# Performance work log

Measured on AMD Instinct MI355X. Metric: run time of the kernel, lower is better.

The kernel has to match this reference:

```python
import jax, jax.numpy as jnp
import numpy as np

N = 20000      # nodes
E = 320000     # edges (avg degree 16)
G = 64         # graphs in batch
D_IN = 771     # input feature dim
H = 256        # hidden dim
L = 5          # message-passing layers


def setup_inputs() -> dict:
    key = jax.random.key(0)
    ks = jax.random.split(key, 20)
    s = 0.05  # weight scale (~xavier magnitude)
    f32 = jnp.float32
    return {
        "x": jax.random.normal(ks[0], (N, D_IN), f32),
        "edge_index": jax.random.randint(ks[1], (2, E), 0, N, dtype=jnp.int32),
        "batch": jnp.sort(jax.random.randint(ks[2], (N,), 0, G, dtype=jnp.int32)),
        # input projection
        "proj_w": jax.random.normal(ks[3], (D_IN, H), f32) * s,
        "proj_b": jnp.zeros((H,), f32),
        # GatedGraphConv per-layer message weights [L, H, H]
        "conv_w": jax.random.normal(ks[4], (L, H, H), f32) * s,
        # GRUCell params (torch layout: [3H, H], gates r,z,n)
        "gru_w_ih": jax.random.normal(ks[5], (3 * H, H), f32) * s,
        "gru_w_hh": jax.random.normal(ks[6], (3 * H, H), f32) * s,
        "gru_b_ih": jnp.zeros((3 * H,), f32),
        "gru_b_hh": jnp.zeros((3 * H,), f32),
        # attention pooling MLP
        "att_w1": jax.random.normal(ks[7], (H, H // 2), f32) * s,
        "att_b1": jnp.zeros((H // 2,), f32),
        "att_w2": jax.random.normal(ks[8], (H // 2, 1), f32) * s,
        "att_b2": jnp.zeros((1,), f32),
        # classifier head
        "cls_w1": jax.random.normal(ks[9], (H, H // 2), f32) * s,
        "cls_b1": jnp.zeros((H // 2,), f32),
        "cls_w2": jax.random.normal(ks[10], (H // 2, 1), f32) * s,
        "cls_b2": jnp.zeros((1,), f32),
    }


def reference(x, edge_index, batch, proj_w, proj_b, conv_w,
              gru_w_ih, gru_w_hh, gru_b_ih, gru_b_hh,
              att_w1, att_b1, att_w2, att_b2,
              cls_w1, cls_b1, cls_w2, cls_b2):
    # input projection (+ReLU); dropout disabled (eval mode)
    h = jax.nn.relu(x @ proj_w + proj_b)  # [N, H]
    src, dst = edge_index[0], edge_index[1]

    def step(h, w_i):
        # per-layer linear message, gather at src, scatter-add at dst
        m = h @ w_i                                         # [N, H]
        agg = jax.ops.segment_sum(m[src], dst, num_segments=N)  # [N, H]
        # GRUCell(agg, h)
        gi = agg @ gru_w_ih.T + gru_b_ih                    # [N, 3H]
        gh = h @ gru_w_hh.T + gru_b_hh                      # [N, 3H]
        i_r, i_z, i_n = jnp.split(gi, 3, axis=-1)
        h_r, h_z, h_n = jnp.split(gh, 3, axis=-1)
        r = jax.nn.sigmoid(i_r + h_r)
        z = jax.nn.sigmoid(i_z + h_z)
        n = jnp.tanh(i_n + r * h_n)
        return (1.0 - z) * n + z * h, None

    h, _ = jax.lax.scan(step, h, conv_w)

    # attention pooling = segment softmax over scores, weighted segment sum
    scores = (jnp.tanh(h @ att_w1 + att_b1) @ att_w2 + att_b2)[:, 0]  # [N]
    smax = jax.ops.segment_max(scores, batch, num_segments=G)         # [G]
    e = jnp.exp(scores - smax[batch])
    denom = jax.ops.segment_sum(e, batch, num_segments=G)
    w = e / denom[batch]
    pooled = jax.ops.segment_sum(h * w[:, None], batch, num_segments=G)  # [G, H]

    out = jax.nn.relu(pooled @ cls_w1 + cls_b1) @ cls_w2 + cls_b2  # [G, 1]
    return out[:, 0]
```

## Files before the change

kernel.cpp:

```cpp
#include <hip/hip_runtime.h>
#include <hip/hip_bf16.h>
#include <math.h>

#define N_NODES 20000
#define M_PAD   20096
#define N_EDGES 320000
#define N_GRAPHS 64
#define D_IN 771
#define KP   800
#define HDIM 256
#define L_LAYERS 5

typedef __attribute__((ext_vector_type(8))) short  bf16x8;
typedef __attribute__((ext_vector_type(8))) unsigned short u16x8;
typedef __attribute__((ext_vector_type(4))) float  f32x4;

typedef __attribute__((address_space(3))) void       lds_void;
typedef __attribute__((address_space(1))) const void gconst_void;

__device__ __forceinline__ void gload16(const void* g, void* l) {
    __builtin_amdgcn_global_load_lds((gconst_void*)g, (lds_void*)l, 16, 0, 0);
}

__device__ __forceinline__ unsigned short f2bf(float f) {
    unsigned int u = __float_as_uint(f);
    return (unsigned short)((u + 0x7FFFu + ((u >> 16) & 1u)) >> 16);
}
__device__ __forceinline__ float bf2f(unsigned short h) {
    return __uint_as_float(((unsigned int)h) << 16);
}

__device__ __forceinline__ int swz_src_elems(int lane, int lr) {
    return ((((lane & 3) * 16) ^ (((lr >> 1) & 3) << 4)) >> 1);
}
__device__ __forceinline__ int swz_read_bytes(int lane, int r) {
    return (((lane >> 4) * 16) ^ (((r >> 1) & 3) << 4));
}

__global__ __launch_bounds__(256)
void prep_x(const float* __restrict__ x, unsigned short* __restrict__ xb) {
    int chunk = blockIdx.x * 256 + threadIdx.x;
    if (chunk >= N_NODES * (KP / 8)) return;
    int r  = chunk / (KP / 8);
    int k0 = (chunk % (KP / 8)) * 8;
    const float* xr = x + (size_t)r * D_IN;
    u16x8 o;
    #pragma unroll
    for (int i = 0; i < 8; i++) {
        int k = k0 + i;
        o[i] = f2bf(k < D_IN ? xr[k] : 0.f);
    }
    *(u16x8*)(xb + (size_t)r * KP + k0) = o;
}
__global__ void prep_projw(const float* __restrict__ w, unsigned short* __restrict__ wt) {
    int i = blockIdx.x * 256 + threadIdx.x;
    if (i >= HDIM * KP) return;
    int n = i / KP, k = i % KP;
    wt[i] = f2bf(k < D_IN ? w[(size_t)k * HDIM + n] : 0.f);
}
__global__ void prep_cast1(const float* __restrict__ a, unsigned short* __restrict__ ab,
                           int n) {
    int i = blockIdx.x * 256 + threadIdx.x;
    if (i < n) ab[i] = f2bf(a[i]);
}

__global__ __launch_bounds__(256)
void weff_gemm(const float* __restrict__ wih, const float* __restrict__ convw,
               unsigned short* __restrict__ weff) {
    __shared__ float As[16][68];
    __shared__ float Bs[16][68];
    const int tid = threadIdx.x;
    const int c0 = blockIdx.x * 64, j0 = blockIdx.y * 64;
    const int l  = blockIdx.z;
    const float* Wc = convw + (size_t)l * HDIM * HDIM;
    const int tm = (tid & 15) * 4, tn = (tid >> 4) * 4;
    const int ar = tid >> 2, ac = (tid & 3) * 4;
    float acc[4][4] = {};
    for (int t0 = 0; t0 < HDIM; t0 += 16) {
        float4 av = *(const float4*)(wih + (size_t)(c0 + ar) * HDIM + t0 + ac);
        float4 bv = *(const float4*)(Wc  + (size_t)(j0 + ar) * HDIM + t0 + ac);
        As[ac + 0][ar] = av.x; As[ac + 1][ar] = av.y;
        As[ac + 2][ar] = av.z; As[ac + 3][ar] = av.w;
        Bs[ac + 0][ar] = bv.x; Bs[ac + 1][ar] = bv.y;
        Bs[ac + 2][ar] = bv.z; Bs[ac + 3][ar] = bv.w;
        __syncthreads();
        #pragma unroll
        for (int kk = 0; kk < 16; kk++) {
            float aa[4] = {As[kk][tm], As[kk][tm+1], As[kk][tm+2], As[kk][tm+3]};
            float bb[4] = {Bs[kk][tn], Bs[kk][tn+1], Bs[kk][tn+2], Bs[kk][tn+3]};
            #pragma unroll
            for (int i = 0; i < 4; i++)
                #pragma unroll
                for (int j = 0; j < 4; j++) acc[i][j] += aa[i] * bb[j];
        }
        __syncthreads();
    }
    #pragma unroll
    for (int i = 0; i < 4; i++)
        #pragma unroll
        for (int j = 0; j < 4; j++)
            weff[(size_t)l * 3 * HDIM * HDIM + (size_t)(c0 + tm + i) * HDIM + j0 + tn + j] =
                f2bf(acc[i][j]);
}

template<int EPI>
__global__ __launch_bounds__(256)
void mm128(const unsigned short* __restrict__ A, int lda,
           const unsigned short* __restrict__ Bt, int ldb,
           const float* __restrict__ bias,
           unsigned short* __restrict__ Cb, int nk) {
    __shared__ char lds[32768];
    const int tid = threadIdx.x;
    const int lane = tid & 63, wave = tid >> 6;
    const int wm = wave >> 1, wn = wave & 1;
    const int row0 = blockIdx.x * 128, col0 = blockIdx.y * 128;
    const int lr = lane >> 2;
    const int kle = swz_src_elems(lane, lr);

    const unsigned short* sA[2];
    const unsigned short* sB[2];
    #pragma unroll
    for (int j = 0; j < 2; ++j) {
        int c = wave * 2 + j;
        sA[j] = A  + (size_t)(row0 + c * 16 + lr) * lda + kle;
        sB[j] = Bt + (size_t)(col0 + c * 16 + lr) * ldb + kle;
    }

    f32x4 acc[4][4];
    #pragma unroll
    for (int i = 0; i < 4; i++)
        #pragma unroll
        for (int j = 0; j < 4; j++) acc[i][j] = (f32x4){0.f, 0.f, 0.f, 0.f};

    auto stage = [&](int buf, int ks) {
        #pragma unroll
        for (int j = 0; j < 2; ++j) {
            int c = wave * 2 + j;
            gload16(sA[j] + ks * 32, lds + buf * 16384 + c * 1024);
            gload16(sB[j] + ks * 32, lds + buf * 16384 + 8192 + c * 1024);
        }
    };

    stage(0, 0);
    __syncthreads();
    for (int ks = 0; ks < nk; ++ks) {
        const int cur = ks & 1;
        if (ks + 1 < nk) stage(cur ^ 1, ks + 1);
        char* L = lds + cur * 16384;
        bf16x8 af[4], bfr[4];
        #pragma unroll
        for (int f = 0; f < 4; ++f) {
            int r = wm * 64 + f * 16 + (lane & 15);
            af[f] = *(const bf16x8*)(L + r * 64 + swz_read_bytes(lane, r));
            int cb = wn * 64 + f * 16 + (lane & 15);
            bfr[f] = *(const bf16x8*)(L + 8192 + cb * 64 + swz_read_bytes(lane, cb));
        }
        #pragma unroll
        for (int i = 0; i < 4; i++)
            #pragma unroll
            for (int j = 0; j < 4; j++)
                acc[i][j] = __builtin_amdgcn_mfma_f32_16x16x32_bf16(af[i], bfr[j], acc[i][j], 0, 0, 0);
        if (ks + 1 < nk) __syncthreads();
    }
    #pragma unroll
    for (int i = 0; i < 4; i++) {
        #pragma unroll
        for (int j = 0; j < 4; j++) {
            int cc = col0 + wn * 64 + j * 16 + (lane & 15);
            #pragma unroll
            for (int ri = 0; ri < 4; ++ri) {
                int rr = row0 + wm * 64 + i * 16 + (lane >> 4) * 4 + ri;
                float v = acc[i][j][ri];
                if (EPI == 1) { v += bias[cc]; v = fmaxf(v, 0.f); }
                Cb[(size_t)rr * HDIM + cc] = f2bf(v);
            }
        }
    }
}

template<int FINAL>
__global__ __launch_bounds__(256, 3)
void gru_mfma(const unsigned short* __restrict__ aggb, const unsigned short* __restrict__ hb,
              const unsigned short* __restrict__ wih, const unsigned short* __restrict__ whh,
              const float* __restrict__ bih, const float* __restrict__ bhh,
              float* __restrict__ hfN, unsigned short* __restrict__ hbN) {
    __shared__ char lds[32768];
    const int tid = threadIdx.x;
    const int lane = tid & 63, wave = tid >> 6;
    const int wm = wave >> 1, wn = wave & 1;
    const int row0 = blockIdx.x * 64, col0 = blockIdx.y * 64;
    const int lr = lane >> 2;
    const int laneoff = lr * HDIM + swz_src_elems(lane, lr);

    const unsigned short* srcs[8];
    #pragma unroll
    for (int j = 0; j < 8; ++j) {
        int c = wave * 8 + j;
        const unsigned short* p;
        int uo;
        if (c < 4)      { p = aggb; uo = (row0 + c * 16) * HDIM; }
        else if (c < 8) { p = hb;   uo = (row0 + (c - 4) * 16) * HDIM; }
        else {
            int t = (c - 8) >> 2, c4 = (c - 8) & 3;
            int s = t >> 1;
            p = (t & 1) ? whh : wih;
            uo = (s * HDIM + col0 + c4 * 16) * HDIM;
        }
        uo = __builtin_amdgcn_readfirstlane(uo);
        srcs[j] = p + uo + laneoff;
    }

    f32x4 acc[3][2][2][2];
    #pragma unroll
    for (int s = 0; s < 3; s++)
        #pragma unroll
        for (int m = 0; m < 2; m++)
            #pragma unroll
            for (int i = 0; i < 2; i++)
                #pragma unroll
                for (int j = 0; j < 2; j++) acc[s][m][i][j] = (f32x4){0.f, 0.f, 0.f, 0.f};

    for (int ks = 0; ks < 8; ++ks) {
        #pragma unroll
        for (int j = 0; j < 8; ++j)
            gload16(srcs[j] + ks * 32, lds + (wave * 8 + j) * 1024);
        __syncthreads();
        bf16x8 a[2][2];
        #pragma unroll
        for (int m = 0; m < 2; m++)
            #pragma unroll
            for (int fr = 0; fr < 2; fr++) {
                int r = wm * 32 + fr * 16 + (lane & 15);
                a[m][fr] = *(const bf16x8*)(lds + m * 4096 + r * 64 + swz_read_bytes(lane, r));
            }
        #pragma unroll
        for (int s = 0; s < 3; s++) {
            bf16x8 b[2][2];
            #pragma unroll
            for (int m = 0; m < 2; m++)
                #pragma unroll
                for (int fc = 0; fc < 2; fc++) {
                    int rb = wn * 32 + fc * 16 + (lane & 15);
                    b[m][fc] = *(const bf16x8*)(lds + 8192 + (s * 2 + m) * 4096 + rb * 64 +
                                                swz_read_bytes(lane, rb));
                }
            #pragma unroll
            for (int m = 0; m < 2; m++)
                #pragma unroll
                for (int fr = 0; fr < 2; fr++)
                    #pragma unroll
                    for (int fc = 0; fc < 2; fc++)
                        acc[s][m][fr][fc] = __builtin_amdgcn_mfma_f32_16x16x32_bf16(
                            a[m][fr], b[m][fc], acc[s][m][fr][fc], 0, 0, 0);
        }
        if (ks < 7) __syncthreads();
    }
    #pragma unroll
    for (int fr = 0; fr < 2; fr++)
        #pragma unroll
        for (int fc = 0; fc < 2; fc++) {
            int cc = col0 + wn * 32 + fc * 16 + (lane & 15);
            float bir = bih[cc],            bhr = bhh[cc];
            float biz = bih[HDIM + cc],     bhz = bhh[HDIM + cc];
            float bin = bih[2 * HDIM + cc], bhn = bhh[2 * HDIM + cc];
            #pragma unroll
            for (int ri = 0; ri < 4; ++ri) {
                int rr = row0 + wm * 32 + fr * 16 + (lane >> 4) * 4 + ri;
                float xr = acc[0][0][fr][fc][ri] + bir + acc[0][1][fr][fc][ri] + bhr;
                float xz = acc[1][0][fr][fc][ri] + biz + acc[1][1][fr][fc][ri] + bhz;
                float gn = acc[2][0][fr][fc][ri] + bin;
                float hn = acc[2][1][fr][fc][ri] + bhn;
                float r_ = 1.f / (1.f + expf(-xr));
                float z_ = 1.f / (1.f + expf(-xz));
                float n_ = tanhf(gn + r_ * hn);
                float ho = bf2f(hb[(size_t)rr * HDIM + cc]);
                float v  = (1.f - z_) * n_ + z_ * ho;
                if (FINAL) hfN[(size_t)rr * HDIM + cc] = v;
                hbN[(size_t)rr * HDIM + cc] = f2bf(v);
            }
        }
}

__global__ void edge_count(const int* __restrict__ ei, int* __restrict__ deg, int E) {
    int e = blockIdx.x * 256 + threadIdx.x;
    if (e < E) atomicAdd(&deg[ei[E + e]], 1);
}
__global__ __launch_bounds__(1024)
void scan_rowptr(const int* __restrict__ deg, int* __restrict__ rowptr, int N) {
    __shared__ int bs[1024];
    const int tid = threadIdx.x;
    const int CH = (N + 1023) / 1024;
    const int base = tid * CH;
    int sum = 0;
    for (int i = 0; i < CH; i++) { int idx = base + i; sum += (idx < N) ? deg[idx] : 0; }
    bs[tid] = sum; __syncthreads();
    for (int off = 1; off < 1024; off <<= 1) {
        int v = (tid >= off) ? bs[tid - off] : 0;
        __syncthreads();
        bs[tid] += v;
        __syncthreads();
    }
    int run = (tid > 0) ? bs[tid - 1] : 0;
    for (int i = 0; i < CH; i++) {
        int idx = base + i;
        if (idx < N) { rowptr[idx] = run; run += deg[idx]; }
    }
    if (tid == 0) rowptr[N] = bs[1023];
}
__global__ void edge_bucket(const int* __restrict__ ei, int* __restrict__ cursor,
                            int* __restrict__ csrc, int E) {
    int e = blockIdx.x * 256 + threadIdx.x;
    if (e < E) {
        int d = ei[E + e];
        int p = atomicAdd(&cursor[d], 1);
        csrc[p] = ei[e];
    }
}

__global__ __launch_bounds__(256)
void agg_bf16(const unsigned short* __restrict__ m, const int* __restrict__ rowptr,
              const int* __restrict__ csrc, unsigned short* __restrict__ agg, int N) {
    int wv = (blockIdx.x * 256 + threadIdx.x) >> 6;
    int lane = threadIdx.x & 63;
    if (wv >= N) return;
    const int half = lane >> 5, l32 = lane & 31;
    int s0 = rowptr[wv], s1 = rowptr[wv + 1];
    float a[8] = {};
    int e = s0 + half;
    for (; e + 2 < s1; e += 4) {
        int sA = csrc[e], sB = csrc[e + 2];
        u16x8 vA = *(const u16x8*)(m + (size_t)sA * HDIM + l32 * 8);
        u16x8 vB = *(const u16x8*)(m + (size_t)sB * HDIM + l32 * 8);
        #pragma unroll
        for (int i = 0; i < 8; i++) a[i] += bf2f(vA[i]) + bf2f(vB[i]);
    }
    for (; e < s1; e += 2) {
        int sA = csrc[e];
        u16x8 vA = *(const u16x8*)(m + (size_t)sA * HDIM + l32 * 8);
        #pragma unroll
        for (int i = 0; i < 8; i++) a[i] += bf2f(vA[i]);
    }
    #pragma unroll
    for (int i = 0; i < 8; i++) a[i] += __shfl_xor(a[i], 32);
    if (half == 0) {
        u16x8 o;
        #pragma unroll
        for (int i = 0; i < 8; i++) o[i] = f2bf(a[i]);
        *(u16x8*)(agg + (size_t)wv * HDIM + l32 * 8) = o;
    }
}

__global__ void seg_starts(const int* __restrict__ batch, int* __restrict__ starts,
                           int N, int G) {
    int n = blockIdx.x * 256 + threadIdx.x;
    if (n > N) return;
    int b  = (n < N) ? batch[n] : G;
    int bp = (n == 0) ? -1 : batch[n - 1];
    for (int g = bp + 1; g <= b; g++) starts[g] = n;
}

__global__ __launch_bounds__(256)
void att_scores2(const float* __restrict__ h, const float* __restrict__ w1,
                 const float* __restrict__ b1, const float* __restrict__ w2,
                 const float* __restrict__ b2, float* __restrict__ scores) {
    __shared__ float As[16][68];
    __shared__ float Bs[16][136];
    __shared__ float red[64][17];
    const int tid = threadIdx.x;
    const int row0 = blockIdx.x * 64;
    const int tm = (tid & 15) * 4, tn = (tid >> 4) * 8;
    const int ar = tid >> 2, ac = (tid & 3) * 4;
    const int br = tid >> 4, bc = (tid & 15) * 8;
    float acc[4][8] = {};
    for (int k0 = 0; k0 < HDIM; k0 += 16) {
        float4 av = {0.f, 0.f, 0.f, 0.f};
        int arow = row0 + ar;
        if (arow < N_NODES) av = *(const float4*)(h + (size_t)arow * HDIM + k0 + ac);
        As[ac + 0][ar] = av.x; As[ac + 1][ar] = av.y;
        As[ac + 2][ar] = av.z; As[ac + 3][ar] = av.w;
        *(float4*)&Bs[br][bc]     = *(const float4*)(w1 + (size_t)(k0 + br) * 128 + bc);
        *(float4*)&Bs[br][bc + 4] = *(const float4*)(w1 + (size_t)(k0 + br) * 128 + bc + 4);
        __syncthreads();
        #pragma unroll
        for (int kk = 0; kk < 16; kk++) {
            float4 a4 = *(const float4*)&As[kk][tm];
            float4 b4 = *(const float4*)&Bs[kk][tn];
            float4 c4 = *(const float4*)&Bs[kk][tn + 4];
            float aa[4] = {a4.x, a4.y, a4.z, a4.w};
            float bb[8] = {b4.x, b4.y, b4.z, b4.w, c4.x, c4.y, c4.z, c4.w};
            #pragma unroll
            for (int i = 0; i < 4; i++)
                #pragma unroll
                for (int j = 0; j < 8; j++) acc[i][j] += aa[i] * bb[j];
        }
        __syncthreads();
    }
    #pragma unroll
    for (int i = 0; i < 4; i++) {
        float s = 0.f;
        #pragma unroll
        for (int j = 0; j < 8; j++)
            s += tanhf(acc[i][j] + b1[tn + j]) * w2[tn + j];
        red[tm + i][tid >> 4] = s;
    }
    __syncthreads();
    if (tid < 64) {
        float s = 0.f;
        #pragma unroll
        for (int g = 0; g < 16; g++) s += red[tid][g];
        int n = row0 + tid;
        if (n < N_NODES) scores[n] = s + b2[0];
    }
}

__global__ __launch_bounds__(256)
void seg_stats(const float* __restrict__ scores, const int* __restrict__ starts,
               float* __restrict__ gmax, float* __restrict__ gden) {
    int wv = (blockIdx.x * 256 + threadIdx.x) >> 6;
    int lane = threadIdx.x & 63;
    if (wv >= N_GRAPHS) return;
    int s0 = starts[wv], s1 = starts[wv + 1];
    float mx = -1e30f;
    for (int n = s0 + lane; n < s1; n += 64) mx = fmaxf(mx, scores[n]);
    #pragma unroll
    for (int off = 32; off > 0; off >>= 1) mx = fmaxf(mx, __shfl_xor(mx, off));
    float se = 0.f;
    for (int n = s0 + lane; n < s1; n += 64) se += expf(scores[n] - mx);
    #pragma unroll
    for (int off = 32; off > 0; off >>= 1) se += __shfl_xor(se, off);
    if (lane == 0) { gmax[wv] = mx; gden[wv] = se; }
}

__global__ void node_weights(const float* __restrict__ scores, const int* __restrict__ batch,
                             const float* __restrict__ gmax, const float* __restrict__ gden,
                             float* __restrict__ wn) {
    int n = blockIdx.x * 256 + threadIdx.x;
    if (n >= N_NODES) return;
    int g = batch[n];
    float d = gden[g];
    wn[n] = (d > 0.f) ? expf(scores[n] - gmax[g]) / d : 0.f;
}

__global__ __launch_bounds__(256)
void pool_partial(const float* __restrict__ h, const float* __restrict__ wn,
                  const int* __restrict__ starts, float* __restrict__ part) {
    int g = blockIdx.x, s = blockIdx.y, tid = threadIdx.x;
    int s0 = starts[g], s1 = starts[g + 1];
    float acc = 0.f;
    for (int n = s0 + s; n < s1; n += 4)
        acc += wn[n] * h[(size_t)n * HDIM + tid];
    part[((size_t)(g * 4 + s)) * HDIM + tid] = acc;
}
__global__ __launch_bounds__(256)
void pool_reduce(const float* __restrict__ part, float* __restrict__ pooled) {
    int g = blockIdx.x, tid = threadIdx.x;
    float s = 0.f;
    #pragma unroll
    for (int i = 0; i < 4; i++) s += part[((size_t)(g * 4 + i)) * HDIM + tid];
    pooled[g * HDIM + tid] = s;
}

__global__ __launch_bounds__(128)
void classify(const float* __restrict__ pooled, const float* __restrict__ w1,
              const float* __restrict__ b1, const float* __restrict__ w2,
              const float* __restrict__ b2, float* __restrict__ out) {
    int g = blockIdx.x;
    int tid = threadIdx.x;
    float acc = 0.f;
    for (int k = 0; k < HDIM; k++) acc += pooled[g * HDIM + k] * w1[k * 128 + tid];
    float t = fmaxf(acc + b1[tid], 0.f);
    float v = t * w2[tid];
    __shared__ float red[128];
    red[tid] = v; __syncthreads();
    for (int off = 64; off > 0; off >>= 1) {
        if (tid < off) red[tid] += red[tid + off];
        __syncthreads();
    }
    if (tid == 0) out[g] = red[0] + b2[0];
}

extern "C" void kernel_launch(void* const* d_in, const int* in_sizes, int n_in,
                              void* d_out, int out_size, void* d_ws, size_t ws_size,
                              hipStream_t stream) {
    const float* x      = (const float*)d_in[0];
    const int*   ei     = (const int*)  d_in[1];
    const int*   batch  = (const int*)  d_in[2];
    const float* proj_w = (const float*)d_in[3];
    const float* proj_b = (const float*)d_in[4];
    const float* conv_w = (const float*)d_in[5];
    const float* w_ih   = (const float*)d_in[6];
    const float* w_hh   = (const float*)d_in[7];
    const float* b_ih   = (const float*)d_in[8];
    const float* b_hh   = (const float*)d_in[9];
    const float* att_w1 = (const float*)d_in[10];
    const float* att_b1 = (const float*)d_in[11];
    const float* att_w2 = (const float*)d_in[12];
    const float* att_b2 = (const float*)d_in[13];
    const float* cls_w1 = (const float*)d_in[14];
    const float* cls_b1 = (const float*)d_in[15];
    const float* cls_w2 = (const float*)d_in[16];
    const float* cls_b2 = (const float*)d_in[17];
    float* out = (float*)d_out;

    char* ws = (char*)d_ws;
    size_t off = 0;
    auto alloc = [&](size_t bytes) -> void* {
        void* p = ws + off;
        off = (off + bytes + 255) & ~(size_t)255;
        return p;
    };
    float*          hfF    = (float*)         alloc((size_t)M_PAD * HDIM * 4);
    unsigned short* hb0    = (unsigned short*)alloc((size_t)M_PAD * HDIM * 2);
    unsigned short* hb1    = (unsigned short*)alloc((size_t)M_PAD * HDIM * 2);
    unsigned short* whhb   = (unsigned short*)alloc((size_t)3 * HDIM * HDIM * 2);
    unsigned short* weffb  = (unsigned short*)alloc((size_t)L_LAYERS * 3 * HDIM * HDIM * 2);
    unsigned short* projWT = (unsigned short*)alloc((size_t)HDIM * KP * 2);
    int*   rowptr = (int*)  alloc((N_NODES + 1) * 4);
    int*   cursor = (int*)  alloc((N_NODES + 1) * 4);
    int*   deg    = (int*)  alloc(N_NODES * 4);
    int*   csrc   = (int*)  alloc(N_EDGES * 4);
    float* scores = (float*)alloc(N_NODES * 4);
    int*   starts = (int*)  alloc((N_GRAPHS + 1) * 4);
    float* gmax   = (float*)alloc(N_GRAPHS * 4);
    float* gden   = (float*)alloc(N_GRAPHS * 4);
    float* wnode  = (float*)alloc(N_NODES * 4);
    float* ppart  = (float*)alloc((size_t)N_GRAPHS * 4 * HDIM * 4);
    float* pooled = (float*)alloc((size_t)N_GRAPHS * HDIM * 4);
    char* U = (char*)alloc((size_t)M_PAD * KP * 2);
    unsigned short* xb   = (unsigned short*)U;
    unsigned short* aggb = (unsigned short*)U;
    (void)ws_size; (void)in_sizes; (void)n_in; (void)out_size;

    prep_x     <<<dim3((N_NODES * (KP / 8) + 255) / 256), dim3(256), 0, stream>>>(x, xb);
    prep_projw <<<dim3((HDIM * KP) / 256), dim3(256), 0, stream>>>(proj_w, projWT);
    prep_cast1 <<<dim3((3 * HDIM * HDIM) / 256), dim3(256), 0, stream>>>(
        w_hh, whhb, 3 * HDIM * HDIM);
    weff_gemm<<<dim3(12, 4, L_LAYERS), dim3(256), 0, stream>>>(w_ih, conv_w, weffb);

    mm128<1><<<dim3(M_PAD / 128, 2), dim3(256), 0, stream>>>(
        xb, KP, projWT, KP, proj_b, hb0, KP / 32);

    hipMemsetAsync(deg, 0, N_NODES * 4, stream);
    edge_count<<<dim3((N_EDGES + 255) / 256), dim3(256), 0, stream>>>(ei, deg, N_EDGES);
    scan_rowptr<<<dim3(1), dim3(1024), 0, stream>>>(deg, rowptr, N_NODES);
    hipMemcpyAsync(cursor, rowptr, (N_NODES + 1) * 4, hipMemcpyDeviceToDevice, stream);
    edge_bucket<<<dim3((N_EDGES + 255) / 256), dim3(256), 0, stream>>>(ei, cursor, csrc, N_EDGES);
    seg_starts<<<dim3((N_NODES + 256) / 256), dim3(256), 0, stream>>>(batch, starts,
                                                                      N_NODES, N_GRAPHS);

    unsigned short* hbc = hb0;  unsigned short* hbn = hb1;
    for (int l = 0; l < L_LAYERS; l++) {
        agg_bf16<<<dim3((N_NODES * 64) / 256), dim3(256), 0, stream>>>(
            hbc, rowptr, csrc, aggb, N_NODES);
        if (l < L_LAYERS - 1)
            gru_mfma<0><<<dim3(M_PAD / 64, 4), dim3(256), 0, stream>>>(
                aggb, hbc, weffb + (size_t)l * 3 * HDIM * HDIM, whhb,
                b_ih, b_hh, nullptr, hbn);
        else
            gru_mfma<1><<<dim3(M_PAD / 64, 4), dim3(256), 0, stream>>>(
                aggb, hbc, weffb + (size_t)l * 3 * HDIM * HDIM, whhb,
                b_ih, b_hh, hfF, hbn);
        unsigned short* tb = hbc; hbc = hbn; hbn = tb;
    }

    att_scores2<<<dim3((N_NODES + 63) / 64), dim3(256), 0, stream>>>(
        hfF, att_w1, att_b1, att_w2, att_b2, scores);
    seg_stats<<<dim3((N_GRAPHS * 64 + 255) / 256), dim3(256), 0, stream>>>(
        scores, starts, gmax, gden);
    node_weights<<<dim3((N_NODES + 255) / 256), dim3(256), 0, stream>>>(
        scores, batch, gmax, gden, wnode);
    pool_partial<<<dim3(N_GRAPHS, 4), dim3(256), 0, stream>>>(hfF, wnode, starts, ppart);
    pool_reduce<<<dim3(N_GRAPHS), dim3(256), 0, stream>>>(ppart, pooled);
    classify<<<dim3(N_GRAPHS), dim3(128), 0, stream>>>(pooled, cls_w1, cls_b1,
                                                       cls_w2, cls_b2, out);
}
```

Baseline: 529.0 us.

## Restructure GRU MFMA kernel into double-buffered 16-step K loop with shared accumulators

The GRU GEMM now treats the input and hidden halves as one concatenated K dimension of 16 steps. The r and z gates accumulate into a single register set, and only the n gate keeps separate input and hidden accumulators. LDS is split into two 16KB buffers so the next K slice is loaded while the current one is multiplied. This cuts accumulator registers from 24 to 16 fragments and overlaps global loads with MFMA work, in exchange for more loop iterations and barriers. The first operand is renamed weff, which suggests the host now passes a pre-combined weight, but no host-side change appears here.

```diff
diff --git a/kernel.cpp b/kernel.cpp
--- a/kernel.cpp
+++ b/kernel.cpp
@@ -181,7 +181,7 @@
 template<int FINAL>
 __global__ __launch_bounds__(256, 3)
 void gru_mfma(const unsigned short* __restrict__ aggb, const unsigned short* __restrict__ hb,
-              const unsigned short* __restrict__ wih, const unsigned short* __restrict__ whh,
+              const unsigned short* __restrict__ weff, const unsigned short* __restrict__ whh,
               const float* __restrict__ bih, const float* __restrict__ bhh,
               float* __restrict__ hfN, unsigned short* __restrict__ hbN) {
     __shared__ char lds[32768];
@@ -192,84 +192,110 @@
     const int lr = lane >> 2;
     const int laneoff = lr * HDIM + swz_src_elems(lane, lr);
 
-    const unsigned short* srcs[8];
-    #pragma unroll
-    for (int j = 0; j < 8; ++j) {
-        int c = wave * 8 + j;
-        const unsigned short* p;
+    const unsigned short* p0[4];
+    const unsigned short* p1[4];
+    #pragma unroll
+    for (int j = 0; j < 4; ++j) {
+        const unsigned short *q0, *q1;
         int uo;
-        if (c < 4)      { p = aggb; uo = (row0 + c * 16) * HDIM; }
-        else if (c < 8) { p = hb;   uo = (row0 + (c - 4) * 16) * HDIM; }
+        if (wave == 0) { q0 = aggb; q1 = hb; uo = (row0 + j * 16) * HDIM; }
         else {
-            int t = (c - 8) >> 2, c4 = (c - 8) & 3;
-            int s = t >> 1;
-            p = (t & 1) ? whh : wih;
-            uo = (s * HDIM + col0 + c4 * 16) * HDIM;
+            int s = wave - 1;
+            q0 = weff; q1 = whh;
+            uo = (s * HDIM + col0 + j * 16) * HDIM;
         }
         uo = __builtin_amdgcn_readfirstlane(uo);
-        srcs[j] = p + uo + laneoff;
-    }
-
-    f32x4 acc[3][2][2][2];
-    #pragma unroll
-    for (int s = 0; s < 3; s++)
-        #pragma unroll
-        for (int m = 0; m < 2; m++)
+        p0[j] = q0 + uo + laneoff;
+        p1[j] = q1 + uo + laneoff;
+    }
+
+    f32x4 accR[2][2], accZ[2][2], accNI[2][2], accNH[2][2];
+    #pragma unroll
+    for (int i = 0; i < 2; i++)
+        #pragma unroll
+        for (int j = 0; j < 2; j++) {
+            accR[i][j] = (f32x4){0.f, 0.f, 0.f, 0.f};
+            accZ[i][j] = (f32x4){0.f, 0.f, 0.f, 0.f};
+            accNI[i][j] = (f32x4){0.f, 0.f, 0.f, 0.f};
+            accNH[i][j] = (f32x4){0.f, 0.f, 0.f, 0.f};
+        }
+
+    auto stage = [&](int buf, int gks) {
+        #pragma unroll
+        for (int j = 0; j < 4; ++j) {
+            const unsigned short* s = (gks < 8 ? p0[j] : p1[j]) + (gks & 7) * 32;
+            gload16(s, lds + buf * 16384 + (wave * 4 + j) * 1024);
+        }
+    };
+
+    stage(0, 0);
+    __syncthreads();
+    for (int ks = 0; ks < 8; ++ks) {
+        const int cur = ks & 1;
+        stage(cur ^ 1, ks + 1);
+        char* L = lds + cur * 16384;
+        bf16x8 a[2], br[2], bz[2], bn[2];
+        #pragma unroll
+        for (int f = 0; f < 2; ++f) {
+            int r = wm * 32 + f * 16 + (lane & 15);
+            a[f] = *(const bf16x8*)(L + r * 64 + swz_read_bytes(lane, r));
+            int rb = wn * 32 + f * 16 + (lane & 15);
+            int so = rb * 64 + swz_read_bytes(lane, rb);
+            br[f] = *(const bf16x8*)(L + 4096 + so);
+            bz[f] = *(const bf16x8*)(L + 8192 + so);
+            bn[f] = *(const bf16x8*)(L + 12288 + so);
+        }
+        #pragma unroll
+        for (int fr = 0; fr < 2; fr++)
             #pragma unroll
-            for (int i = 0; i < 2; i++)
-                #pragma unroll
-                for (int j = 0; j < 2; j++) acc[s][m][i][j] = (f32x4){0.f, 0.f, 0.f, 0.f};
-
-    for (int ks = 0; ks < 8; ++ks) {
-        #pragma unroll
-        for (int j = 0; j < 8; ++j)
-            gload16(srcs[j] + ks * 32, lds + (wave * 8 + j) * 1024);
-        __syncthreads();
-        bf16x8 a[2][2];
-        #pragma unroll
-        for (int m = 0; m < 2; m++)
+            for (int fc = 0; fc < 2; fc++) {
+                accR[fr][fc]  = __builtin_amdgcn_mfma_f32_16x16x32_bf16(a[fr], br[fc], accR[fr][fc], 0, 0, 0);
+                accZ[fr][fc]  = __builtin_amdgcn_mfma_f32_16x16x32_bf16(a[fr], bz[fc], accZ[fr][fc], 0, 0, 0);
+                accNI[fr][fc] = __builtin_amdgcn_mfma_f32_16x16x32_bf16(a[fr], bn[fc], accNI[fr][fc], 0, 0, 0);
+            }
+        __syncthreads();
+    }
+    for (int ks = 8; ks < 16; ++ks) {
+        const int cur = ks & 1;
+        if (ks < 15) stage(cur ^ 1, ks + 1);
+        char* L = lds + cur * 16384;
+        bf16x8 a[2], br[2], bz[2], bn[2];
+        #pragma unroll
+        for (int f = 0; f < 2; ++f) {
+            int r = wm * 32 + f * 16 + (lane & 15);
+            a[f] = *(const bf16x8*)(L + r * 64 + swz_read_bytes(lane, r));
+            int rb = wn * 32 + f * 16 + (lane & 15);
+            int so = rb * 64 + swz_read_bytes(lane, rb);
+            br[f] = *(const bf16x8*)(L + 4096 + so);
+            bz[f] = *(const bf16x8*)(L + 8192 + so);
+            bn[f] = *(const bf16x8*)(L + 12288 + so);
+        }
+        #pragma unroll
+        for (int fr = 0; fr < 2; fr++)
             #pragma unroll
-            for (int fr = 0; fr < 2; fr++) {
-                int r = wm * 32 + fr * 16 + (lane & 15);
-                a[m][fr] = *(const bf16x8*)(lds + m * 4096 + r * 64 + swz_read_bytes(lane, r));
+            for (int fc = 0; fc < 2; fc++) {
+                accR[fr][fc]  = __builtin_amdgcn_mfma_f32_16x16x32_bf16(a[fr], br[fc], accR[fr][fc], 0, 0, 0);
+                accZ[fr][fc]  = __builtin_amdgcn_mfma_f32_16x16x32_bf16(a[fr], bz[fc], accZ[fr][fc], 0, 0, 0);
+                accNH[fr][fc] = __builtin_amdgcn_mfma_f32_16x16x32_bf16(a[fr], bn[fc], accNH[fr][fc], 0, 0, 0);
             }
-        #pragma unroll
-        for (int s = 0; s < 3; s++) {
-            bf16x8 b[2][2];
-            #pragma unroll
-            for (int m = 0; m < 2; m++)
-                #pragma unroll
-                for (int fc = 0; fc < 2; fc++) {
-                    int rb = wn * 32 + fc * 16 + (lane & 15);
-                    b[m][fc] = *(const bf16x8*)(lds + 8192 + (s * 2 + m) * 4096 + rb * 64 +
-                                                swz_read_bytes(lane, rb));
-                }
-            #pragma unroll
-            for (int m = 0; m < 2; m++)
-                #pragma unroll
-                for (int fr = 0; fr < 2; fr++)
-                    #pragma unroll
-                    for (int fc = 0; fc < 2; fc++)
-                        acc[s][m][fr][fc] = __builtin_amdgcn_mfma_f32_16x16x32_bf16(
-                            a[m][fr], b[m][fc], acc[s][m][fr][fc], 0, 0, 0);
-        }
-        if (ks < 7) __syncthreads();
+        if (ks < 15) __syncthreads();
     }
     #pragma unroll
     for (int fr = 0; fr < 2; fr++)
         #pragma unroll
         for (int fc = 0; fc < 2; fc++) {
             int cc = col0 + wn * 32 + fc * 16 + (lane & 15);
-            float bir = bih[cc],            bhr = bhh[cc];
-            float biz = bih[HDIM + cc],     bhz = bhh[HDIM + cc];
-            float bin = bih[2 * HDIM + cc], bhn = bhh[2 * HDIM + cc];
+            float brz = bih[cc]            + bhh[cc];
+            float bzz = bih[HDIM + cc]     + bhh[HDIM + cc];
+            float bin = bih[2 * HDIM + cc];
+            float bhn = bhh[2 * HDIM + cc];
             #pragma unroll
             for (int ri = 0; ri < 4; ++ri) {
                 int rr = row0 + wm * 32 + fr * 16 + (lane >> 4) * 4 + ri;
-                float xr = acc[0][0][fr][fc][ri] + bir + acc[0][1][fr][fc][ri] + bhr;
-                float xz = acc[1][0][fr][fc][ri] + biz + acc[1][1][fr][fc][ri] + bhz;
-                float gn = acc[2][0][fr][fc][ri] + bin;
-                float hn = acc[2][1][fr][fc][ri] + bhn;
+                float xr = accR[fr][fc][ri] + brz;
+                float xz = accZ[fr][fc][ri] + bzz;
+                float gn = accNI[fr][fc][ri] + bin;
+                float hn = accNH[fr][fc][ri] + bhn;
                 float r_ = 1.f / (1.f + expf(-xr));
                 float z_ = 1.f / (1.f + expf(-xz));
                 float n_ = tanhf(gn + r_ * hn);
```

New measurement: 532.4 us. No clear change (+0.6%).
